# Kernel optimization log

Measured on AMD Instinct MI355X. Metric: run time of the kernel, lower is better.

The kernel has to match this reference:

```python
import jax, jax.numpy as jnp
import numpy as np

EMBED = 512
HEADS = 8
HEAD_DIM = EMBED // HEADS
LN_EPS = 1e-5


def setup_inputs() -> dict:
    key = jax.random.key(0)
    ks = jax.random.split(key, 13)
    B, L = 4, 2048
    s = 1.0 / np.sqrt(EMBED)
    inp = {
        "values": jax.random.normal(ks[0], (B, L, EMBED), dtype=jnp.float32),
        "keys": jax.random.normal(ks[1], (B, L, EMBED), dtype=jnp.float32),
        "query": jax.random.normal(ks[2], (B, L, EMBED), dtype=jnp.float32),
        "Wq": jax.random.uniform(ks[3], (EMBED, EMBED), jnp.float32, -s, s),
        "bq": jax.random.uniform(ks[4], (EMBED,), jnp.float32, -s, s),
        "Wk": jax.random.uniform(ks[5], (EMBED, EMBED), jnp.float32, -s, s),
        "bk": jax.random.uniform(ks[6], (EMBED,), jnp.float32, -s, s),
        "Wv": jax.random.uniform(ks[7], (EMBED, EMBED), jnp.float32, -s, s),
        "bv": jax.random.uniform(ks[8], (EMBED,), jnp.float32, -s, s),
        "Wo": jax.random.uniform(ks[9], (EMBED, EMBED), jnp.float32, -s, s),
        "bo": jax.random.uniform(ks[10], (EMBED,), jnp.float32, -s, s),
        "ln_g": jnp.ones((EMBED,), jnp.float32),
        "ln_b": jnp.zeros((EMBED,), jnp.float32),
    }
    return inp


def reference(values, keys, query, Wq, bq, Wk, bk, Wv, bv, Wo, bo, ln_g, ln_b):
    B, L, _ = query.shape
    # separate QKV linears (torch Linear: x @ W^T + b)
    Q = (query @ Wq.T + bq).reshape(B, L, HEADS, HEAD_DIM)
    K = (keys @ Wk.T + bk).reshape(B, L, HEADS, HEAD_DIM)
    V = (values @ Wv.T + bv).reshape(B, L, HEADS, HEAD_DIM)
    # explicit QK^T scores: [B, H, Q, K]
    scores = jnp.einsum("nqhd,nkhd->nhqk", Q, K) / np.sqrt(HEAD_DIM)
    attn = jax.nn.softmax(scores, axis=-1)
    out = jnp.einsum("nhqk,nkhd->nqhd", attn, V).reshape(B, L, EMBED)
    out = out @ Wo.T + bo
    # residual + LayerNorm (dropout = identity in eval)
    x = out + query
    mu = jnp.mean(x, axis=-1, keepdims=True)
    var = jnp.var(x, axis=-1, keepdims=True)
    return (x - mu) * jax.lax.rsqrt(var + LN_EPS) * ln_g + ln_b
```

## Files before the change

kernel.cpp:

```cpp
#include <hip/hip_runtime.h>

typedef short bf16x8 __attribute__((ext_vector_type(8)));
typedef short s16x4 __attribute__((ext_vector_type(4)));
typedef float f32x4 __attribute__((ext_vector_type(4)));
typedef unsigned int uint4v __attribute__((ext_vector_type(4)));
typedef unsigned int uint2v __attribute__((ext_vector_type(2)));

#define BLM   8192
#define EMB   512
#define LSEQ  2048
#define NHEAD 8
#define HDIM  64

typedef __attribute__((address_space(3))) char lds_ch;

__device__ __forceinline__ unsigned short f2bf(float x) {
    unsigned int u = __builtin_bit_cast(unsigned int, x);
    u += 0x7FFFu + ((u >> 16) & 1u);
    return (unsigned short)(u >> 16);
}

__device__ __forceinline__ unsigned int cvtpk(float lo, float hi) {
    unsigned int r;
    asm("v_cvt_pk_bf16_f32 %0, %1, %2" : "=v"(r) : "v"(lo), "v"(hi));
    return r;
}

__device__ __forceinline__ int swz(int row, int bcol) {
    return row * 128 + (bcol ^ ((row & 7) << 4));
}

#define GLL16(g, l) __builtin_amdgcn_global_load_lds( \
    (const __attribute__((address_space(1))) void*)(g), \
    (__attribute__((address_space(3))) void*)(l), 16, 0, 0)

#define TR16(dst, a, OFF) asm volatile("ds_read_b64_tr_b16 %0, %1 offset:%2" \
    : "=v"(dst) : "v"(a), "n"(OFF))

__global__ __launch_bounds__(256, 3) void k_gemm_qkv(
    const float* __restrict__ Xq, const float* __restrict__ Xk, const float* __restrict__ Xv,
    const float* __restrict__ Wq, const float* __restrict__ Wk, const float* __restrict__ Wv,
    const float* __restrict__ bq, const float* __restrict__ bk, const float* __restrict__ bv,
    unsigned short* __restrict__ Qb, unsigned short* __restrict__ Kb, unsigned short* __restrict__ Vb)
{
    const int z = blockIdx.z;
    const float* X    = (z == 0) ? Xq : (z == 1) ? Xk : Xv;
    const float* W    = (z == 0) ? Wq : (z == 1) ? Wk : Wv;
    const float* bias = (z == 0) ? bq : (z == 1) ? bk : bv;
    unsigned short* out = (z == 0) ? Qb : (z == 1) ? Kb : Vb;
    const float osc = (z == 0) ? 0.125f * 1.44269504088896340736f : 1.0f;

    __shared__ __align__(16) char lds[32768];
    char* As = lds;
    char* Bs = lds + 16384;

    const int tid  = threadIdx.x;
    const int lane = tid & 63;
    const int wave = tid >> 6;
    const int wm = wave >> 1, wn = wave & 1;
    const int lr = lane & 15, lk = lane >> 4;
    const int m0 = blockIdx.x * 128, n0 = blockIdx.y * 128;

    f32x4 acc[4][4] = {};

    const float* pa = X + (size_t)(m0 + (tid >> 4)) * EMB + (tid & 15) * 4;
    const float* pb = W + (size_t)(n0 + (tid >> 4)) * EMB + (tid & 15) * 4;

    float4 ar[8], br[8];
    #pragma unroll
    for (int i = 0; i < 8; ++i) {
        ar[i] = *(const float4*)(pa + (size_t)i * 16 * EMB);
        br[i] = *(const float4*)(pb + (size_t)i * 16 * EMB);
    }
    pa += 64; pb += 64;

    for (int kt = 0; kt < 8; ++kt) {
        __syncthreads();
        #pragma unroll
        for (int i = 0; i < 8; ++i) {
            int f = tid + i * 256;
            int r = f >> 4, c4 = f & 15;
            uint2v p; p.x = cvtpk(ar[i].x, ar[i].y); p.y = cvtpk(ar[i].z, ar[i].w);
            *(uint2v*)(As + swz(r, c4 * 8)) = p;
            uint2v q; q.x = cvtpk(br[i].x, br[i].y); q.y = cvtpk(br[i].z, br[i].w);
            *(uint2v*)(Bs + swz(r, c4 * 8)) = q;
        }
        if (kt < 7) {
            #pragma unroll
            for (int i = 0; i < 8; ++i) {
                ar[i] = *(const float4*)(pa + (size_t)i * 16 * EMB);
                br[i] = *(const float4*)(pb + (size_t)i * 16 * EMB);
            }
            pa += 64; pb += 64;
        }
        __syncthreads();
        #pragma unroll
        for (int ks = 0; ks < 2; ++ks) {
            bf16x8 af[4], bfr[4];
            #pragma unroll
            for (int fm = 0; fm < 4; ++fm)
                af[fm] = *(const bf16x8*)(As + swz(wm * 64 + fm * 16 + lr, ks * 64 + lk * 16));
            #pragma unroll
            for (int fn = 0; fn < 4; ++fn)
                bfr[fn] = *(const bf16x8*)(Bs + swz(wn * 64 + fn * 16 + lr, ks * 64 + lk * 16));
            #pragma unroll
            for (int fm = 0; fm < 4; ++fm)
                #pragma unroll
                for (int fn = 0; fn < 4; ++fn)
                    acc[fm][fn] = __builtin_amdgcn_mfma_f32_16x16x32_bf16(af[fm], bfr[fn], acc[fm][fn], 0, 0, 0);
        }
    }
    #pragma unroll
    for (int fn = 0; fn < 4; ++fn) {
        int n = n0 + wn * 64 + fn * 16 + lr;
        float bv_ = bias[n];
        #pragma unroll
        for (int fm = 0; fm < 4; ++fm) {
            int mb = m0 + wm * 64 + fm * 16 + lk * 4;
            #pragma unroll
            for (int j = 0; j < 4; ++j)
                out[(size_t)(mb + j) * EMB + n] = f2bf((acc[fm][fn][j] + bv_) * osc);
        }
    }
}

__global__ __launch_bounds__(256, 3) void k_gemm_out(
    const unsigned short* __restrict__ AO, const float* __restrict__ Wo,
    const float* __restrict__ bo, const float* __restrict__ res,
    float* __restrict__ Xout)
{
    __shared__ __align__(16) char lds[32768];
    char* As = lds;
    char* Bs = lds + 16384;

    const int tid  = threadIdx.x;
    const int lane = tid & 63;
    const int wave = tid >> 6;
    const int wm = wave >> 1, wn = wave & 1;
    const int lr = lane & 15, lk = lane >> 4;
    const int m0 = blockIdx.x * 128, n0 = blockIdx.y * 128;

    f32x4 acc[4][4] = {};

    const unsigned short* pA = AO + (size_t)(m0 + (tid >> 3)) * EMB + (tid & 7) * 8;
    const float* pB = Wo + (size_t)(n0 + (tid >> 4)) * EMB + (tid & 15) * 4;

    uint4v arA[4]; float4 brB[8];
    #pragma unroll
    for (int i = 0; i < 4; ++i) arA[i] = *(const uint4v*)(pA + (size_t)i * 32 * EMB);
    #pragma unroll
    for (int i = 0; i < 8; ++i) brB[i] = *(const float4*)(pB + (size_t)i * 16 * EMB);
    pA += 64; pB += 64;

    for (int kt = 0; kt < 8; ++kt) {
        __syncthreads();
        #pragma unroll
        for (int i = 0; i < 4; ++i) {
            int f = tid + i * 256;
            int r = f >> 3, c8 = f & 7;
            *(uint4v*)(As + swz(r, c8 * 16)) = arA[i];
        }
        #pragma unroll
        for (int i = 0; i < 8; ++i) {
            int f = tid + i * 256;
            int r = f >> 4, c4 = f & 15;
            uint2v q; q.x = cvtpk(brB[i].x, brB[i].y); q.y = cvtpk(brB[i].z, brB[i].w);
            *(uint2v*)(Bs + swz(r, c4 * 8)) = q;
        }
        if (kt < 7) {
            #pragma unroll
            for (int i = 0; i < 4; ++i) arA[i] = *(const uint4v*)(pA + (size_t)i * 32 * EMB);
            #pragma unroll
            for (int i = 0; i < 8; ++i) brB[i] = *(const float4*)(pB + (size_t)i * 16 * EMB);
            pA += 64; pB += 64;
        }
        __syncthreads();
        #pragma unroll
        for (int ks = 0; ks < 2; ++ks) {
            bf16x8 af[4], bfr[4];
            #pragma unroll
            for (int fm = 0; fm < 4; ++fm)
                af[fm] = *(const bf16x8*)(As + swz(wm * 64 + fm * 16 + lr, ks * 64 + lk * 16));
            #pragma unroll
            for (int fn = 0; fn < 4; ++fn)
                bfr[fn] = *(const bf16x8*)(Bs + swz(wn * 64 + fn * 16 + lr, ks * 64 + lk * 16));
            #pragma unroll
            for (int fm = 0; fm < 4; ++fm)
                #pragma unroll
                for (int fn = 0; fn < 4; ++fn)
                    acc[fm][fn] = __builtin_amdgcn_mfma_f32_16x16x32_bf16(af[fm], bfr[fn], acc[fm][fn], 0, 0, 0);
        }
    }
    #pragma unroll
    for (int fn = 0; fn < 4; ++fn) {
        int n = n0 + wn * 64 + fn * 16 + lr;
        float bv_ = bo[n];
        #pragma unroll
        for (int fm = 0; fm < 4; ++fm) {
            int mb = m0 + wm * 64 + fm * 16 + lk * 4;
            #pragma unroll
            for (int j = 0; j < 4; ++j) {
                size_t idx = (size_t)(mb + j) * EMB + n;
                Xout[idx] = acc[fm][fn][j] + bv_ + res[idx];
            }
        }
    }
}

__global__ __launch_bounds__(512, 4) void k_attn(
    const unsigned short* __restrict__ Qb, const unsigned short* __restrict__ Kb,
    const unsigned short* __restrict__ Vb, unsigned short* __restrict__ AO)
{
    __shared__ __align__(16) char lds[65536];
    lds_ch* LB = (lds_ch*)lds;

    const int tid  = threadIdx.x;
    const int lane = tid & 63;
    const int wave = tid >> 6;
    const int lr = lane & 15, lk = lane >> 4;

    const int bh = blockIdx.y;
    const int b = bh >> 3, h = bh & 7;
    const size_t base = (size_t)b * LSEQ * EMB + h * HDIM;
    const int q0 = blockIdx.x * 128 + wave * 16;

    const int c0 = tid, c1 = tid + 512;
    auto kcol = [](int c) { int r = c >> 3; return ((c & 7) * 8) ^ ((r & 7) * 8); };
    const unsigned short* srcK0 = Kb + base + (size_t)(c0 >> 3) * EMB + kcol(c0);
    const unsigned short* srcK1 = Kb + base + (size_t)(c1 >> 3) * EMB + kcol(c1);
    auto vsrc = [&](int c) {
        int kv = ((c >> 3) & 31) * 4 + ((c >> 1) & 3);
        int d  = (c >> 8) * 16 + (c & 1) * 8;
        return Vb + base + (size_t)kv * EMB + d;
    };
    const unsigned short* srcV0 = vsrc(c0);
    const unsigned short* srcV1 = vsrc(c1);

    auto stage = [&](int par) {
        lds_ch* kd = LB + par * 16384 + wave * 1024;
        lds_ch* vd = LB + 32768 + par * 16384 + wave * 1024;
        GLL16(srcK0, kd);
        GLL16(srcK1, kd + 8192);
        GLL16(srcV0, vd);
        GLL16(srcV1, vd + 8192);
        srcK0 += 128 * EMB; srcK1 += 128 * EMB;
        srcV0 += 128 * EMB; srcV1 += 128 * EMB;
    };

    bf16x8 qf[2];
    #pragma unroll
    for (int ks = 0; ks < 2; ++ks)
        qf[ks] = *(const bf16x8*)(Qb + base + (size_t)(q0 + lr) * EMB + ks * 32 + lk * 8);

    f32x4 oaccT[4] = {};
    float lrow = 0.f;

    lds_ch* vadB = LB + 32768 + lk * 128 + lr * 2;

    stage(0);

    for (int t = 0; t < 16; ++t) {
        const int par = t & 1;
        __syncthreads();
        if (t < 15) stage(par ^ 1);

        char* Kl = lds + par * 16384;
        f32x4 sacc[8] = {};
        __builtin_amdgcn_s_setprio(1);
        #pragma unroll
        for (int ks = 0; ks < 2; ++ks) {
            bf16x8 kf[8];
            #pragma unroll
            for (int blk = 0; blk < 8; ++blk)
                kf[blk] = *(const bf16x8*)(Kl + swz(blk * 16 + lr, ks * 64 + lk * 16));
            #pragma unroll
            for (int blk = 0; blk < 8; ++blk)
                sacc[blk] = __builtin_amdgcn_mfma_f32_16x16x32_bf16(kf[blk], qf[ks], sacc[blk], 0, 0, 0);
        }
        __builtin_amdgcn_s_setprio(0);

        #pragma unroll
        for (int blk = 0; blk < 8; ++blk)
            #pragma unroll
            for (int j = 0; j < 4; ++j)
                sacc[blk][j] = __builtin_amdgcn_exp2f(sacc[blk][j]);
        f32x4 ps0 = sacc[0] + sacc[1];
        f32x4 ps1 = sacc[2] + sacc[3];
        f32x4 ps2 = sacc[4] + sacc[5];
        f32x4 ps3 = sacc[6] + sacc[7];
        f32x4 ps  = (ps0 + ps1) + (ps2 + ps3);
        lrow += (ps[0] + ps[1]) + (ps[2] + ps[3]);

        bf16x8 pf[4];
        #pragma unroll
        for (int k = 0; k < 4; ++k) {
            uint4v w;
            w.x = cvtpk(sacc[2 * k][0],     sacc[2 * k][1]);
            w.y = cvtpk(sacc[2 * k][2],     sacc[2 * k][3]);
            w.z = cvtpk(sacc[2 * k + 1][0], sacc[2 * k + 1][1]);
            w.w = cvtpk(sacc[2 * k + 1][2], sacc[2 * k + 1][3]);
            pf[k] = __builtin_bit_cast(bf16x8, w);
        }

        lds_ch* vad = vadB + par * 16384;
        __builtin_amdgcn_s_setprio(1);
        #pragma unroll
        for (int fd = 0; fd < 4; ++fd) {
            uint2v t0, t1, t2, t3, t4, t5, t6, t7;
            TR16(t0, vad, 0);    TR16(t1, vad, 512);
            TR16(t2, vad, 1024); TR16(t3, vad, 1536);
            TR16(t4, vad, 2048); TR16(t5, vad, 2560);
            TR16(t6, vad, 3072); TR16(t7, vad, 3584);
            asm volatile("s_waitcnt lgkmcnt(0)" ::: "memory");
            __builtin_amdgcn_sched_barrier(0);
            uint4v w0; w0.x = t0.x; w0.y = t0.y; w0.z = t1.x; w0.w = t1.y;
            uint4v w1; w1.x = t2.x; w1.y = t2.y; w1.z = t3.x; w1.w = t3.y;
            uint4v w2; w2.x = t4.x; w2.y = t4.y; w2.z = t5.x; w2.w = t5.y;
            uint4v w3; w3.x = t6.x; w3.y = t6.y; w3.z = t7.x; w3.w = t7.y;
            oaccT[fd] = __builtin_amdgcn_mfma_f32_16x16x32_bf16(__builtin_bit_cast(bf16x8, w0), pf[0], oaccT[fd], 0, 0, 0);
            oaccT[fd] = __builtin_amdgcn_mfma_f32_16x16x32_bf16(__builtin_bit_cast(bf16x8, w1), pf[1], oaccT[fd], 0, 0, 0);
            oaccT[fd] = __builtin_amdgcn_mfma_f32_16x16x32_bf16(__builtin_bit_cast(bf16x8, w2), pf[2], oaccT[fd], 0, 0, 0);
            oaccT[fd] = __builtin_amdgcn_mfma_f32_16x16x32_bf16(__builtin_bit_cast(bf16x8, w3), pf[3], oaccT[fd], 0, 0, 0);
            vad += 4096;
        }
        __builtin_amdgcn_s_setprio(0);
    }

    lrow += __shfl_xor(lrow, 16);
    lrow += __shfl_xor(lrow, 32);
    float inv = 1.f / lrow;
    unsigned short* aorow = AO + base + (size_t)(q0 + lr) * EMB;
    #pragma unroll
    for (int fd = 0; fd < 4; ++fd) {
        s16x4 s;
        #pragma unroll
        for (int j = 0; j < 4; ++j) s[j] = (short)f2bf(oaccT[fd][j] * inv);
        *(s16x4*)(aorow + fd * 16 + lk * 4) = s;
    }
}

__global__ __launch_bounds__(64) void k_ln(
    const float* __restrict__ X, const float* __restrict__ g,
    const float* __restrict__ bta, float* __restrict__ out)
{
    const int row = blockIdx.x, lane = threadIdx.x;
    const float* x = X + (size_t)row * EMB;
    float4 a = *(const float4*)(x + lane * 8);
    float4 c = *(const float4*)(x + lane * 8 + 4);
    float s  = a.x + a.y + a.z + a.w + c.x + c.y + c.z + c.w;
    float sq = a.x*a.x + a.y*a.y + a.z*a.z + a.w*a.w + c.x*c.x + c.y*c.y + c.z*c.z + c.w*c.w;
    #pragma unroll
    for (int msk = 1; msk < 64; msk <<= 1) { s += __shfl_xor(s, msk); sq += __shfl_xor(sq, msk); }
    float mu  = s * (1.f / 512.f);
    float var = sq * (1.f / 512.f) - mu * mu;
    float rs  = rsqrtf(var + 1e-5f);
    float4 g0 = *(const float4*)(g + lane * 8), g1 = *(const float4*)(g + lane * 8 + 4);
    float4 b0 = *(const float4*)(bta + lane * 8), b1 = *(const float4*)(bta + lane * 8 + 4);
    float4 o0, o1;
    o0.x = (a.x - mu) * rs * g0.x + b0.x;  o0.y = (a.y - mu) * rs * g0.y + b0.y;
    o0.z = (a.z - mu) * rs * g0.z + b0.z;  o0.w = (a.w - mu) * rs * g0.w + b0.w;
    o1.x = (c.x - mu) * rs * g1.x + b1.x;  o1.y = (c.y - mu) * rs * g1.y + b1.y;
    o1.z = (c.z - mu) * rs * g1.z + b1.z;  o1.w = (c.w - mu) * rs * g1.w + b1.w;
    *(float4*)(out + (size_t)row * EMB + lane * 8) = o0;
    *(float4*)(out + (size_t)row * EMB + lane * 8 + 4) = o1;
}

extern "C" void kernel_launch(void* const* d_in, const int* in_sizes, int n_in,
                              void* d_out, int out_size, void* d_ws, size_t ws_size,
                              hipStream_t stream) {
    const float* values = (const float*)d_in[0];
    const float* keys   = (const float*)d_in[1];
    const float* query  = (const float*)d_in[2];
    const float* Wq = (const float*)d_in[3];  const float* bq = (const float*)d_in[4];
    const float* Wk = (const float*)d_in[5];  const float* bk = (const float*)d_in[6];
    const float* Wv = (const float*)d_in[7];  const float* bv = (const float*)d_in[8];
    const float* Wo = (const float*)d_in[9];  const float* bo = (const float*)d_in[10];
    const float* lng = (const float*)d_in[11];
    const float* lnb = (const float*)d_in[12];

    char* ws = (char*)d_ws;
    unsigned short* Qb = (unsigned short*)(ws);
    unsigned short* Kb = (unsigned short*)(ws + 8u  * 1024 * 1024);
    unsigned short* Vb = (unsigned short*)(ws + 16u * 1024 * 1024);
    unsigned short* AO = (unsigned short*)(ws + 24u * 1024 * 1024);
    float*          Xr = (float*)(ws);

    dim3 gqkv(64, 4, 3);
    k_gemm_qkv<<<gqkv, 256, 0, stream>>>(query, keys, values, Wq, Wk, Wv, bq, bk, bv, Qb, Kb, Vb);
    k_attn<<<dim3(16, 32), 512, 0, stream>>>(Qb, Kb, Vb, AO);
    k_gemm_out<<<dim3(64, 4), 256, 0, stream>>>(AO, Wo, bo, query, Xr);
    k_ln<<<8192, 64, 0, stream>>>(Xr, lng, lnb, (float*)d_out);
}
```

Measured before the change: 90.95 us.

## Halve attention block to 4 waves each handling two 16-row query groups

The attention kernel now uses 256-thread blocks where each wave computes two 16-query groups, so every K fragment and transposed V fragment read from LDS feeds two MFMAs instead of one. Each thread issues four async global-to-LDS loads per stage instead of two. The grid becomes 1D with a remapped block index that spreads consecutive blocks across (batch, head) groups, likely for XCD/L2 locality. The trade-off is double the accumulator and score registers per wave and fewer waves per block to hide latency.

New measurement: 88.34 us. -2.9%, faster.

```diff
diff --git a/kernel.cpp b/kernel.cpp
--- a/kernel.cpp
+++ b/kernel.cpp
@@ -207,7 +207,7 @@
     }
 }
 
-__global__ __launch_bounds__(512, 4) void k_attn(
+__global__ __launch_bounds__(256, 2) void k_attn(
     const unsigned short* __restrict__ Qb, const unsigned short* __restrict__ Kb,
     const unsigned short* __restrict__ Vb, unsigned short* __restrict__ AO)
 {
@@ -219,41 +219,39 @@
     const int wave = tid >> 6;
     const int lr = lane & 15, lk = lane >> 4;
 
-    const int bh = blockIdx.y;
+    const int bid  = blockIdx.x;
+    const int orig = (bid & 7) * 64 + (bid >> 3);
+    const int qx = orig & 15, bh = orig >> 4;
     const int b = bh >> 3, h = bh & 7;
     const size_t base = (size_t)b * LSEQ * EMB + h * HDIM;
-    const int q0 = blockIdx.x * 128 + wave * 16;
-
-    const int c0 = tid, c1 = tid + 512;
+    const int q0 = qx * 128 + wave * 32;
+
     auto kcol = [](int c) { int r = c >> 3; return ((c & 7) * 8) ^ ((r & 7) * 8); };
-    const unsigned short* srcK0 = Kb + base + (size_t)(c0 >> 3) * EMB + kcol(c0);
-    const unsigned short* srcK1 = Kb + base + (size_t)(c1 >> 3) * EMB + kcol(c1);
-    auto vsrc = [&](int c) {
-        int kv = ((c >> 3) & 31) * 4 + ((c >> 1) & 3);
-        int d  = (c >> 8) * 16 + (c & 1) * 8;
-        return Vb + base + (size_t)kv * EMB + d;
-    };
-    const unsigned short* srcV0 = vsrc(c0);
-    const unsigned short* srcV1 = vsrc(c1);
+    const unsigned short* srcK = Kb + base + (size_t)(tid >> 3) * EMB + kcol(tid);
+    const unsigned short* srcV = Vb + base
+        + (size_t)(((tid >> 3) & 31) * 4 + ((tid >> 1) & 3)) * EMB + (tid & 1) * 8;
 
     auto stage = [&](int par) {
         lds_ch* kd = LB + par * 16384 + wave * 1024;
         lds_ch* vd = LB + 32768 + par * 16384 + wave * 1024;
-        GLL16(srcK0, kd);
-        GLL16(srcK1, kd + 8192);
-        GLL16(srcV0, vd);
-        GLL16(srcV1, vd + 8192);
-        srcK0 += 128 * EMB; srcK1 += 128 * EMB;
-        srcV0 += 128 * EMB; srcV1 += 128 * EMB;
+        #pragma unroll
+        for (int i = 0; i < 4; ++i) {
+            GLL16(srcK + (size_t)i * 32 * EMB, kd + i * 4096);
+            GLL16(srcV + i * 16,               vd + i * 4096);
+        }
+        srcK += 128 * EMB;
+        srcV += 128 * EMB;
     };
 
-    bf16x8 qf[2];
-    #pragma unroll
-    for (int ks = 0; ks < 2; ++ks)
-        qf[ks] = *(const bf16x8*)(Qb + base + (size_t)(q0 + lr) * EMB + ks * 32 + lk * 8);
-
-    f32x4 oaccT[4] = {};
-    float lrow = 0.f;
+    bf16x8 qf[2][2];
+    #pragma unroll
+    for (int qg = 0; qg < 2; ++qg)
+        #pragma unroll
+        for (int ks = 0; ks < 2; ++ks)
+            qf[qg][ks] = *(const bf16x8*)(Qb + base + (size_t)(q0 + qg * 16 + lr) * EMB + ks * 32 + lk * 8);
+
+    f32x4 oaccT[2][4] = {};
+    float lrow[2] = {0.f, 0.f};
 
     lds_ch* vadB = LB + 32768 + lk * 128 + lr * 2;
 
@@ -265,7 +263,7 @@
         if (t < 15) stage(par ^ 1);
 
         char* Kl = lds + par * 16384;
-        f32x4 sacc[8] = {};
+        f32x4 s0[8] = {}, s1[8] = {};
         __builtin_amdgcn_s_setprio(1);
         #pragma unroll
         for (int ks = 0; ks < 2; ++ks) {
@@ -274,32 +272,46 @@
             for (int blk = 0; blk < 8; ++blk)
                 kf[blk] = *(const bf16x8*)(Kl + swz(blk * 16 + lr, ks * 64 + lk * 16));
             #pragma unroll
-            for (int blk = 0; blk < 8; ++blk)
-                sacc[blk] = __builtin_amdgcn_mfma_f32_16x16x32_bf16(kf[blk], qf[ks], sacc[blk], 0, 0, 0);
+            for (int blk = 0; blk < 8; ++blk) {
+                s0[blk] = __builtin_amdgcn_mfma_f32_16x16x32_bf16(kf[blk], qf[0][ks], s0[blk], 0, 0, 0);
+                s1[blk] = __builtin_amdgcn_mfma_f32_16x16x32_bf16(kf[blk], qf[1][ks], s1[blk], 0, 0, 0);
+            }
         }
         __builtin_amdgcn_s_setprio(0);
 
         #pragma unroll
         for (int blk = 0; blk < 8; ++blk)
             #pragma unroll
-            for (int j = 0; j < 4; ++j)
-                sacc[blk][j] = __builtin_amdgcn_exp2f(sacc[blk][j]);
-        f32x4 ps0 = sacc[0] + sacc[1];
-        f32x4 ps1 = sacc[2] + sacc[3];
-        f32x4 ps2 = sacc[4] + sacc[5];
-        f32x4 ps3 = sacc[6] + sacc[7];
-        f32x4 ps  = (ps0 + ps1) + (ps2 + ps3);
-        lrow += (ps[0] + ps[1]) + (ps[2] + ps[3]);
-
-        bf16x8 pf[4];
+            for (int j = 0; j < 4; ++j) {
+                s0[blk][j] = __builtin_amdgcn_exp2f(s0[blk][j]);
+                s1[blk][j] = __builtin_amdgcn_exp2f(s1[blk][j]);
+            }
+        {
+            f32x4 pa = (s0[0] + s0[1]) + (s0[2] + s0[3]);
+            f32x4 pb = (s0[4] + s0[5]) + (s0[6] + s0[7]);
+            f32x4 pc = pa + pb;
+            lrow[0] += (pc[0] + pc[1]) + (pc[2] + pc[3]);
+            f32x4 qa = (s1[0] + s1[1]) + (s1[2] + s1[3]);
+            f32x4 qb = (s1[4] + s1[5]) + (s1[6] + s1[7]);
+            f32x4 qc = qa + qb;
+            lrow[1] += (qc[0] + qc[1]) + (qc[2] + qc[3]);
+        }
+
+        bf16x8 pf0[4], pf1[4];
         #pragma unroll
         for (int k = 0; k < 4; ++k) {
             uint4v w;
-            w.x = cvtpk(sacc[2 * k][0],     sacc[2 * k][1]);
-            w.y = cvtpk(sacc[2 * k][2],     sacc[2 * k][3]);
-            w.z = cvtpk(sacc[2 * k + 1][0], sacc[2 * k + 1][1]);
-            w.w = cvtpk(sacc[2 * k + 1][2], sacc[2 * k + 1][3]);
-            pf[k] = __builtin_bit_cast(bf16x8, w);
+            w.x = cvtpk(s0[2 * k][0],     s0[2 * k][1]);
+            w.y = cvtpk(s0[2 * k][2],     s0[2 * k][3]);
+            w.z = cvtpk(s0[2 * k + 1][0], s0[2 * k + 1][1]);
+            w.w = cvtpk(s0[2 * k + 1][2], s0[2 * k + 1][3]);
+            pf0[k] = __builtin_bit_cast(bf16x8, w);
+            uint4v v;
+            v.x = cvtpk(s1[2 * k][0],     s1[2 * k][1]);
+            v.y = cvtpk(s1[2 * k][2],     s1[2 * k][3]);
+            v.z = cvtpk(s1[2 * k + 1][0], s1[2 * k + 1][1]);
+            v.w = cvtpk(s1[2 * k + 1][2], s1[2 * k + 1][3]);
+            pf1[k] = __builtin_bit_cast(bf16x8, v);
         }
 
         lds_ch* vad = vadB + par * 16384;
@@ -317,25 +329,37 @@
             uint4v w1; w1.x = t2.x; w1.y = t2.y; w1.z = t3.x; w1.w = t3.y;
             uint4v w2; w2.x = t4.x; w2.y = t4.y; w2.z = t5.x; w2.w = t5.y;
             uint4v w3; w3.x = t6.x; w3.y = t6.y; w3.z = t7.x; w3.w = t7.y;
-            oaccT[fd] = __builtin_amdgcn_mfma_f32_16x16x32_bf16(__builtin_bit_cast(bf16x8, w0), pf[0], oaccT[fd], 0, 0, 0);
-            oaccT[fd] = __builtin_amdgcn_mfma_f32_16x16x32_bf16(__builtin_bit_cast(bf16x8, w1), pf[1], oaccT[fd], 0, 0, 0);
-            oaccT[fd] = __builtin_amdgcn_mfma_f32_16x16x32_bf16(__builtin_bit_cast(bf16x8, w2), pf[2], oaccT[fd], 0, 0, 0);
-            oaccT[fd] = __builtin_amdgcn_mfma_f32_16x16x32_bf16(__builtin_bit_cast(bf16x8, w3), pf[3], oaccT[fd], 0, 0, 0);
+            bf16x8 v0 = __builtin_bit_cast(bf16x8, w0);
+            bf16x8 v1 = __builtin_bit_cast(bf16x8, w1);
+            bf16x8 v2 = __builtin_bit_cast(bf16x8, w2);
+            bf16x8 v3 = __builtin_bit_cast(bf16x8, w3);
+            oaccT[0][fd] = __builtin_amdgcn_mfma_f32_16x16x32_bf16(v0, pf0[0], oaccT[0][fd], 0, 0, 0);
+            oaccT[1][fd] = __builtin_amdgcn_mfma_f32_16x16x32_bf16(v0, pf1[0], oaccT[1][fd], 0, 0, 0);
+            oaccT[0][fd] = __builtin_amdgcn_mfma_f32_16x16x32_bf16(v1, pf0[1], oaccT[0][fd], 0, 0, 0);
+            oaccT[1][fd] = __builtin_amdgcn_mfma_f32_16x16x32_bf16(v1, pf1[1], oaccT[1][fd], 0, 0, 0);
+            oaccT[0][fd] = __builtin_amdgcn_mfma_f32_16x16x32_bf16(v2, pf0[2], oaccT[0][fd], 0, 0, 0);
+            oaccT[1][fd] = __builtin_amdgcn_mfma_f32_16x16x32_bf16(v2, pf1[2], oaccT[1][fd], 0, 0, 0);
+            oaccT[0][fd] = __builtin_amdgcn_mfma_f32_16x16x32_bf16(v3, pf0[3], oaccT[0][fd], 0, 0, 0);
+            oaccT[1][fd] = __builtin_amdgcn_mfma_f32_16x16x32_bf16(v3, pf1[3], oaccT[1][fd], 0, 0, 0);
             vad += 4096;
         }
         __builtin_amdgcn_s_setprio(0);
     }
 
-    lrow += __shfl_xor(lrow, 16);
-    lrow += __shfl_xor(lrow, 32);
-    float inv = 1.f / lrow;
-    unsigned short* aorow = AO + base + (size_t)(q0 + lr) * EMB;
-    #pragma unroll
-    for (int fd = 0; fd < 4; ++fd) {
-        s16x4 s;
-        #pragma unroll
-        for (int j = 0; j < 4; ++j) s[j] = (short)f2bf(oaccT[fd][j] * inv);
-        *(s16x4*)(aorow + fd * 16 + lk * 4) = s;
+    #pragma unroll
+    for (int qg = 0; qg < 2; ++qg) {
+        float lr_ = lrow[qg];
+        lr_ += __shfl_xor(lr_, 16);
+        lr_ += __shfl_xor(lr_, 32);
+        float inv = 1.f / lr_;
+        unsigned short* aorow = AO + base + (size_t)(q0 + qg * 16 + lr) * EMB;
+        #pragma unroll
+        for (int fd = 0; fd < 4; ++fd) {
+            s16x4 s;
+            #pragma unroll
+            for (int j = 0; j < 4; ++j) s[j] = (short)f2bf(oaccT[qg][fd][j] * inv);
+            *(s16x4*)(aorow + fd * 16 + lk * 4) = s;
+        }
     }
 }
 
@@ -387,7 +411,7 @@
 
     dim3 gqkv(64, 4, 3);
     k_gemm_qkv<<<gqkv, 256, 0, stream>>>(query, keys, values, Wq, Wk, Wv, bq, bk, bv, Qb, Kb, Vb);
-    k_attn<<<dim3(16, 32), 512, 0, stream>>>(Qb, Kb, Vb, AO);
+    k_attn<<<512, 256, 0, stream>>>(Qb, Kb, Vb, AO);
     k_gemm_out<<<dim3(64, 4), 256, 0, stream>>>(AO, Wo, bo, query, Xr);
     k_ln<<<8192, 64, 0, stream>>>(Xr, lng, lnb, (float*)d_out);
 }
```
